# Performance work log

Hardware: AMD Instinct MI355X
Metric: run time of the kernel (lower is better)

Reference implementation:

```python
import jax, jax.numpy as jnp
import numpy as np

K_NEIGHBORS = 8  # hard-coded k in extract_edge_features
NUM_HEADS = 12


def _sqdist(a, b):
    # a [B,M,3], b [B,N,3] -> squared euclidean distances [B,M,N]
    # (monotone in cdist, so argmax/top-k indices are identical to torch.cdist)
    return jnp.sum((a[:, :, None, :] - b[:, None, :, :]) ** 2, axis=-1)


def _fps(points, num_samples):
    # Farthest point sampling (intended semantics of farthest_point_sampling):
    # iteratively pick the point maximizing the min distance to the selected set.
    B, N, _ = points.shape
    bidx = jnp.arange(B)

    def d_to(idx):  # idx [B] -> squared dist from points[b, idx[b]] to all points [B,N]
        p = points[bidx, idx]  # [B,3]
        return jnp.sum((points - p[:, None, :]) ** 2, axis=-1)

    idx0 = jnp.zeros((B,), jnp.int32)  # deterministic start point

    def step(min_d, _):
        nxt = jnp.argmax(min_d, axis=-1).astype(jnp.int32)  # [B]
        min_d = jnp.minimum(min_d, d_to(nxt))
        return min_d, nxt

    _, rest = jax.lax.scan(step, d_to(idx0), None, length=num_samples - 1)  # rest [M-1,B]
    idxs = jnp.concatenate([idx0[None, :], rest], axis=0).T  # [B,M]
    return jnp.take_along_axis(points, idxs[:, :, None], axis=1)  # [B,M,3]


def _edge_features(points, features, k=K_NEIGHBORS):
    # EdgeAligner.extract_edge_features: kNN by cdist+topk(smallest), then
    # edge = feature - mean(neighbor features)
    d2 = _sqdist(points, points)  # [B,M,M]
    _, nn_idx = jax.lax.top_k(-d2, k)  # [B,M,k] indices of k nearest (incl. self)
    nbr = jax.vmap(lambda f, idx: f[idx])(features, nn_idx)  # [B,M,k,D]
    return features - jnp.mean(nbr, axis=2)


def _mha(x, Wq, bq, Wk, bk, Wv, bv, Wo, bo, num_heads=NUM_HEADS):
    # standard torch nn.MultiheadAttention (self-attention, batch_first)
    B, S, D = x.shape
    dh = D // num_heads
    split = lambda t: t.reshape(B, S, num_heads, dh).transpose(0, 2, 1, 3)
    q = split(x @ Wq + bq)
    k = split(x @ Wk + bk)
    v = split(x @ Wv + bv)
    scale = jnp.asarray(1.0 / np.sqrt(dh), x.dtype)
    att = jax.nn.softmax(jnp.einsum('bhqd,bhkd->bhqk', q, k) * scale, axis=-1)
    o = jnp.einsum('bhqk,bhkd->bhqd', att, v)  # [B,H,S,dh]
    o = o.transpose(0, 2, 1, 3).reshape(B, S, D)
    return o @ Wo + bo


def setup_inputs() -> dict:
    key = jax.random.key(0)
    ks = jax.random.split(key, 8)
    B, N, D = 4, 8192, 768
    s = 0.02
    return {
        'points': jax.random.normal(ks[0], (B, N, 3), jnp.float32),
        'W_embed': jax.random.normal(ks[1], (3, D), jnp.float32) * s,
        'b_embed': jnp.zeros((D,), jnp.float32),
        'Wq': jax.random.normal(ks[2], (D, D), jnp.float32) * s,
        'bq': jnp.zeros((D,), jnp.float32),
        'Wk': jax.random.normal(ks[3], (D, D), jnp.float32) * s,
        'bk': jnp.zeros((D,), jnp.float32),
        'Wv': jax.random.normal(ks[4], (D, D), jnp.float32) * s,
        'bv': jnp.zeros((D,), jnp.float32),
        'Wo': jax.random.normal(ks[5], (D, D), jnp.float32) * s,
        'bo': jnp.zeros((D,), jnp.float32),
        'Ws': jax.random.normal(ks[6], (3, D), jnp.float32) * s,
        'bs': jnp.zeros((D,), jnp.float32),
        'num_samples': 1024,
    }


def reference(points, W_embed, b_embed, Wq, bq, Wk, bk, Wv, bv, Wo, bo, Ws, bs, num_samples):
    # 1) farthest point sampling N -> M
    sampled = _fps(points, num_samples)  # [B,M,3]
    # 2) point embedding (point_embed: Linear(3, 768))
    feats = sampled @ W_embed + b_embed  # [B,M,768]
    # 3) EdgeAligner forward with no external neighbor subsets:
    #    edge features -> self bi-attention -> + spatial embedding
    edge = _edge_features(sampled, feats)  # [B,M,768]
    aligned = _mha(edge, Wq, bq, Wk, bk, Wv, bv, Wo, bo)  # [B,M,768]
    spatial = sampled @ Ws + bs  # spatial_embed: Linear(3, 768)
    return aligned + spatial
```

## Files before the change

kernel.cpp:

```cpp
#include <hip/hip_runtime.h>
#include <float.h>
#include <math.h>

#define BB   4
#define NPTS 8192
#define MS   1024
#define DIM  768
#define NH   12
#define DHD  64
#define KNN  8
#define BMD  (BB*MS*DIM)

static __device__ __forceinline__ float sqdist3(float ax, float ay, float az,
                                                float bx, float by, float bz) {
  float dx = __fsub_rn(ax, bx);
  float dy = __fsub_rn(ay, by);
  float dz = __fsub_rn(az, bz);
  return __fadd_rn(__fadd_rn(__fmul_rn(dx, dx), __fmul_rn(dy, dy)), __fmul_rn(dz, dz));
}

__global__ __launch_bounds__(1024) void fps_kernel(const float* __restrict__ points,
                                                   float* __restrict__ sampled) {
  const int b = blockIdx.x;
  const float* pts = points + (size_t)b * NPTS * 3;
  float* smp = sampled + (size_t)b * MS * 3;
  const int tid = threadIdx.x;
  const int lane = tid & 63, wid = tid >> 6;

  __shared__ float cxs[NPTS], cys[NPTS], czs[NPTS];
  __shared__ unsigned long long red[2][16];

  float px[8], py[8], pz[8], md[8];
  const float qx0 = pts[0], qy0 = pts[1], qz0 = pts[2];
#pragma unroll
  for (int j = 0; j < 8; ++j) {
    int i = tid + j * 1024;
    float x = pts[i * 3 + 0], y = pts[i * 3 + 1], z = pts[i * 3 + 2];
    px[j] = x; py[j] = y; pz[j] = z;
    cxs[i] = x; cys[i] = y; czs[i] = z;
    md[j] = sqdist3(x, y, z, qx0, qy0, qz0);
  }
  if (tid == 0) { smp[0] = qx0; smp[1] = qy0; smp[2] = qz0; }
  __syncthreads();

  for (int s = 1; s < MS; ++s) {
    float bv = md[0]; int bj = 0;
#pragma unroll
    for (int j = 1; j < 8; ++j)
      if (md[j] > bv) { bv = md[j]; bj = j; }
    unsigned long long key =
        ((unsigned long long)__float_as_uint(bv) << 32) |
        (unsigned)(~(unsigned)(tid + bj * 1024));

#pragma unroll
    for (int off = 1; off < 64; off <<= 1) {
      unsigned long long ok = __shfl_xor(key, off);
      if (ok > key) key = ok;
    }
    const int buf = s & 1;
    if (lane == 0) red[buf][wid] = key;
    __syncthreads();

    unsigned long long kk[16];
#pragma unroll
    for (int i = 0; i < 16; ++i) kk[i] = red[buf][i];
#pragma unroll
    for (int st = 8; st >= 1; st >>= 1)
#pragma unroll
      for (int i = 0; i < 8; ++i)
        if (i < st && kk[i + st] > kk[i]) kk[i] = kk[i + st];

    const unsigned widx = ~(unsigned)(kk[0] & 0xffffffffull);
    const float wx = cxs[widx], wy = cys[widx], wz = czs[widx];
    if (tid == 0) {
      smp[s * 3 + 0] = wx; smp[s * 3 + 1] = wy; smp[s * 3 + 2] = wz;
    }
#pragma unroll
    for (int j = 0; j < 8; ++j) {
      float d = sqdist3(px[j], py[j], pz[j], wx, wy, wz);
      md[j] = fminf(md[j], d);
    }
  }
}

__global__ void embed_kernel(const float* __restrict__ sampled,
                             const float* __restrict__ W,
                             const float* __restrict__ bias,
                             float* __restrict__ out) {
  int idx = blockIdx.x * blockDim.x + threadIdx.x;
  if (idx >= BMD) return;
  int d = idx % DIM;
  int bm = idx / DIM;
  float x = sampled[bm * 3 + 0], y = sampled[bm * 3 + 1], z = sampled[bm * 3 + 2];
  out[idx] = fmaf(z, W[2 * DIM + d], fmaf(y, W[DIM + d], fmaf(x, W[d], bias[d])));
}

__global__ __launch_bounds__(256) void knn_edge_kernel(const float* __restrict__ sampled,
                                                       const float* __restrict__ feats,
                                                       float* __restrict__ edge) {
  const int bm = blockIdx.x;
  const int b = bm >> 10, m = bm & 1023;
  const float* sp = sampled + (size_t)b * MS * 3;
  const int t = threadIdx.x, lane = t & 63, wid = t >> 6;

  __shared__ float dist[MS];
  __shared__ float redv[4];
  __shared__ int   redi[4];
  __shared__ int   win[KNN];

  const float qx = sp[m * 3 + 0], qy = sp[m * 3 + 1], qz = sp[m * 3 + 2];
#pragma unroll
  for (int j = 0; j < 4; ++j) {
    int i = t + j * 256;
    dist[i] = sqdist3(sp[i * 3 + 0], sp[i * 3 + 1], sp[i * 3 + 2], qx, qy, qz);
  }
  __syncthreads();

  for (int it = 0; it < KNN; ++it) {
    float bv = dist[t]; int bi = t;
#pragma unroll
    for (int j = 1; j < 4; ++j) {
      int i = t + j * 256;
      float v = dist[i];
      if (v < bv || (v == bv && i < bi)) { bv = v; bi = i; }
    }
#pragma unroll
    for (int off = 32; off >= 1; off >>= 1) {
      float ov = __shfl_xor(bv, off);
      int   oi = __shfl_xor(bi, off);
      if (ov < bv || (ov == bv && oi < bi)) { bv = ov; bi = oi; }
    }
    if (lane == 0) { redv[wid] = bv; redi[wid] = bi; }
    __syncthreads();
    if (t == 0) {
      float wv = redv[0]; int wi = redi[0];
#pragma unroll
      for (int w = 1; w < 4; ++w) {
        float ov = redv[w]; int oi = redi[w];
        if (ov < wv || (ov == wv && oi < wi)) { wv = ov; wi = oi; }
      }
      win[it] = wi;
      dist[wi] = FLT_MAX;
    }
    __syncthreads();
  }

  const float* fb = feats + (size_t)b * MS * DIM;
  float* eb = edge + (size_t)b * MS * DIM;
  for (int d = t; d < DIM; d += 256) {
    float acc = 0.f;
#pragma unroll
    for (int i = 0; i < KNN; ++i) acc += fb[(size_t)win[i] * DIM + d];
    eb[(size_t)m * DIM + d] = fb[(size_t)m * DIM + d] - acc * 0.125f;
  }
}

template <int MODE>
__global__ __launch_bounds__(256) void gemm_kernel(const float* __restrict__ A,
                                                   const float* __restrict__ W,
                                                   const float* __restrict__ bias,
                                                   float* __restrict__ C,
                                                   const float* __restrict__ sampled,
                                                   const float* __restrict__ Ws,
                                                   const float* __restrict__ bs) {
  __shared__ float As[16][68];
  __shared__ float Bs[16][68];

  const int t = threadIdx.x;
  const int tx = t & 15, ty = t >> 4;
  const int rowBase = blockIdx.x * 64;
  const int nBase = blockIdx.y * 64;

  float c[4][4] = {};

  const int ar = t >> 2, ac4 = (t & 3) * 4;
  const int br = t >> 4, bc4 = (t & 15) * 4;

  for (int k0 = 0; k0 < DIM; k0 += 16) {
    float4 a = *(const float4*)&A[(size_t)(rowBase + ar) * DIM + k0 + ac4];
    As[ac4 + 0][ar] = a.x; As[ac4 + 1][ar] = a.y;
    As[ac4 + 2][ar] = a.z; As[ac4 + 3][ar] = a.w;
    float4 w = *(const float4*)&W[(size_t)(k0 + br) * DIM + nBase + bc4];
    *(float4*)&Bs[br][bc4] = w;
    __syncthreads();
#pragma unroll
    for (int k = 0; k < 16; ++k) {
      float av[4], bv[4];
      *(float4*)av = *(const float4*)&As[k][ty * 4];
      *(float4*)bv = *(const float4*)&Bs[k][tx * 4];
#pragma unroll
      for (int i = 0; i < 4; ++i)
#pragma unroll
        for (int j = 0; j < 4; ++j)
          c[i][j] = fmaf(av[i], bv[j], c[i][j]);
    }
    __syncthreads();
  }

#pragma unroll
  for (int i = 0; i < 4; ++i) {
    int row = rowBase + ty * 4 + i;
#pragma unroll
    for (int j = 0; j < 4; ++j) {
      int n = nBase + tx * 4 + j;
      float v = c[i][j] + bias[n];
      if (MODE == 1) {
        const float* sp = sampled + (size_t)row * 3;
        float spt = fmaf(sp[2], Ws[2 * DIM + n], fmaf(sp[1], Ws[DIM + n], fmaf(sp[0], Ws[n], bs[n])));
        v += spt;
      }
      C[(size_t)row * DIM + n] = v;
    }
  }
}

static __device__ __forceinline__ int lidx(int r, int c) {
  return r * 64 + (c ^ ((r & 7) << 2));
}

__global__ __launch_bounds__(256) void attn_kernel(const float* __restrict__ Q,
                                                   const float* __restrict__ K,
                                                   const float* __restrict__ V,
                                                   float* __restrict__ O) {
  const int nrt = MS / 64;
  const int blk = blockIdx.x;
  const int bh = blk / nrt, rt = blk % nrt;
  const int b = bh / NH, h = bh % NH;
  const int t = threadIdx.x, lane = t & 63, w = t >> 6;
  const int rg = lane >> 4, kg = lane & 15;

  __shared__ float Qs[64 * 64];
  __shared__ float Ks[64 * 64];
  __shared__ float Vs[64 * 64];
  __shared__ float Ps[4 * 16 * 64];

  const size_t base = (size_t)(b * MS) * DIM + (size_t)h * DHD;

#pragma unroll
  for (int i = 0; i < 4; ++i) {
    int f = t + i * 256;
    int r = f >> 4, c4 = (f & 15) * 4;
    *(float4*)&Qs[lidx(r, c4)] = *(const float4*)&Q[base + (size_t)(rt * 64 + r) * DIM + c4];
  }

  float m[4], l[4], o[4][4];
#pragma unroll
  for (int i = 0; i < 4; ++i) {
    m[i] = -INFINITY; l[i] = 0.f;
#pragma unroll
    for (int j = 0; j < 4; ++j) o[i][j] = 0.f;
  }

  const int lrow = w * 16 + rg * 4;
  float* Pw = &Ps[w * 16 * 64];

  for (int kt = 0; kt < nrt; ++kt) {
#pragma unroll
    for (int i = 0; i < 4; ++i) {
      int f = t + i * 256;
      int r = f >> 4, c4 = (f & 15) * 4;
      size_t g = base + (size_t)(kt * 64 + r) * DIM + c4;
      *(float4*)&Ks[lidx(r, c4)] = *(const float4*)&K[g];
      *(float4*)&Vs[lidx(r, c4)] = *(const float4*)&V[g];
    }
    __syncthreads();

    float s[4][4] = {};
#pragma unroll 8
    for (int d = 0; d < 64; ++d) {
      float a[4], bb[4];
#pragma unroll
      for (int i = 0; i < 4; ++i) a[i] = Qs[lidx(lrow + i, d)];
#pragma unroll
      for (int j = 0; j < 4; ++j) bb[j] = Ks[lidx(kg + 16 * j, d)];
#pragma unroll
      for (int i = 0; i < 4; ++i)
#pragma unroll
        for (int j = 0; j < 4; ++j) s[i][j] = fmaf(a[i], bb[j], s[i][j]);
    }

#pragma unroll
    for (int i = 0; i < 4; ++i) {
#pragma unroll
      for (int j = 0; j < 4; ++j) s[i][j] *= 0.125f;
      float mt = fmaxf(fmaxf(s[i][0], s[i][1]), fmaxf(s[i][2], s[i][3]));
#pragma unroll
      for (int off = 1; off < 16; off <<= 1) mt = fmaxf(mt, __shfl_xor(mt, off));
      float mn = fmaxf(m[i], mt);
      float corr = expf(m[i] - mn);
      float ps = 0.f;
#pragma unroll
      for (int j = 0; j < 4; ++j) { s[i][j] = expf(s[i][j] - mn); ps += s[i][j]; }
#pragma unroll
      for (int off = 1; off < 16; off <<= 1) ps += __shfl_xor(ps, off);
      l[i] = l[i] * corr + ps;
      m[i] = mn;
#pragma unroll
      for (int j = 0; j < 4; ++j) o[i][j] *= corr;
#pragma unroll
      for (int j = 0; j < 4; ++j) Pw[lidx(rg * 4 + i, kg + 16 * j)] = s[i][j];
    }

#pragma unroll 8
    for (int k = 0; k < 64; ++k) {
      float a[4], bb[4];
#pragma unroll
      for (int i = 0; i < 4; ++i) a[i] = Pw[lidx(rg * 4 + i, k)];
#pragma unroll
      for (int j = 0; j < 4; ++j) bb[j] = Vs[lidx(k, kg + 16 * j)];
#pragma unroll
      for (int i = 0; i < 4; ++i)
#pragma unroll
        for (int j = 0; j < 4; ++j) o[i][j] = fmaf(a[i], bb[j], o[i][j]);
    }
    __syncthreads();
  }

#pragma unroll
  for (int i = 0; i < 4; ++i) {
    int row = rt * 64 + lrow + i;
#pragma unroll
    for (int j = 0; j < 4; ++j)
      O[base + (size_t)row * DIM + kg + 16 * j] = o[i][j] / l[i];
  }
}

extern "C" void kernel_launch(void* const* d_in, const int* in_sizes, int n_in,
                              void* d_out, int out_size, void* d_ws, size_t ws_size,
                              hipStream_t stream) {
  const float* points  = (const float*)d_in[0];
  const float* W_embed = (const float*)d_in[1];
  const float* b_embed = (const float*)d_in[2];
  const float* Wq = (const float*)d_in[3];
  const float* bq = (const float*)d_in[4];
  const float* Wk = (const float*)d_in[5];
  const float* bk = (const float*)d_in[6];
  const float* Wv = (const float*)d_in[7];
  const float* bv = (const float*)d_in[8];
  const float* Wo = (const float*)d_in[9];
  const float* bo = (const float*)d_in[10];
  const float* Ws = (const float*)d_in[11];
  const float* bs = (const float*)d_in[12];

  float* ws = (float*)d_ws;
  float* sampled = ws;
  float* feats   = ws + 16384;
  float* edge    = feats + BMD;
  float* qb      = edge + BMD;
  float* kb      = qb + BMD;
  float* vb      = kb + BMD;
  float* ao      = vb + BMD;

  fps_kernel<<<BB, 1024, 0, stream>>>(points, sampled);
  embed_kernel<<<(BMD + 255) / 256, 256, 0, stream>>>(sampled, W_embed, b_embed, feats);
  knn_edge_kernel<<<BB * MS, 256, 0, stream>>>(sampled, feats, edge);

  dim3 ggrid(4096 / 64, DIM / 64);
  gemm_kernel<0><<<ggrid, 256, 0, stream>>>(edge, Wq, bq, qb, nullptr, nullptr, nullptr);
  gemm_kernel<0><<<ggrid, 256, 0, stream>>>(edge, Wk, bk, kb, nullptr, nullptr, nullptr);
  gemm_kernel<0><<<ggrid, 256, 0, stream>>>(edge, Wv, bv, vb, nullptr, nullptr, nullptr);

  attn_kernel<<<BB * NH * (MS / 64), 256, 0, stream>>>(qb, kb, vb, ao);

  gemm_kernel<1><<<ggrid, 256, 0, stream>>>(ao, Wo, bo, (float*)d_out, sampled, Ws, bs);
}
```

Before: 2.091 ms.

## Shrink FPS block to 4 waves with DPP reductions, enlarge GEMM row tile

The farthest-point-sampling kernel now runs 256 threads per batch, each holding 32 points. The argmax is fused into the distance-update loop, and the wave reduction uses DPP row/broadcast ops instead of shuffles. Coordinates are packed as float4 in shared memory, and the cross-wave reduction shrinks from 16 entries to 4, which cuts per-iteration barrier and reduction latency on the serial 1023-step loop. Separately, the generic GEMM tile grows from 64x64 to 128x64 with an 8x4 per-thread micro-tile. This halves the grid and raises register use for more reuse per load.

Result: faster. 1.833 ms (-12.4%).

```diff
diff --git a/kernel.cpp b/kernel.cpp
--- a/kernel.cpp
+++ b/kernel.cpp
@@ -19,66 +19,82 @@
   return __fadd_rn(__fadd_rn(__fmul_rn(dx, dx), __fmul_rn(dy, dy)), __fmul_rn(dz, dz));
 }
 
-__global__ __launch_bounds__(1024) void fps_kernel(const float* __restrict__ points,
-                                                   float* __restrict__ sampled) {
+#define DPP_STAGE(key, ctrl)                                                   \
+  {                                                                            \
+    unsigned hi_ = (unsigned)((key) >> 32), lo_ = (unsigned)(key);             \
+    unsigned nhi_ = (unsigned)__builtin_amdgcn_update_dpp(                     \
+        (int)hi_, (int)hi_, (ctrl), 0xf, 0xf, false);                          \
+    unsigned nlo_ = (unsigned)__builtin_amdgcn_update_dpp(                     \
+        (int)lo_, (int)lo_, (ctrl), 0xf, 0xf, false);                          \
+    unsigned long long nk_ = ((unsigned long long)nhi_ << 32) | nlo_;          \
+    if (nk_ > (key)) (key) = nk_;                                              \
+  }
+
+__global__ __launch_bounds__(256, 1) void fps_kernel(const float* __restrict__ points,
+                                                     float* __restrict__ sampled) {
   const int b = blockIdx.x;
   const float* pts = points + (size_t)b * NPTS * 3;
   float* smp = sampled + (size_t)b * MS * 3;
   const int tid = threadIdx.x;
-  const int lane = tid & 63, wid = tid >> 6;
-
-  __shared__ float cxs[NPTS], cys[NPTS], czs[NPTS];
-  __shared__ unsigned long long red[2][16];
-
-  float px[8], py[8], pz[8], md[8];
+  const int lane = tid & 63, w = tid >> 6;
+
+  __shared__ float4 cxyz[NPTS];
+  __shared__ unsigned long long red[2][4];
+
+  float px[32], py[32], pz[32], md[32];
   const float qx0 = pts[0], qy0 = pts[1], qz0 = pts[2];
-#pragma unroll
-  for (int j = 0; j < 8; ++j) {
-    int i = tid + j * 1024;
+
+  float bv = -INFINITY;
+  int bidx = 0;
+#pragma unroll
+  for (int j = 0; j < 32; ++j) {
+    int i = tid + j * 256;
     float x = pts[i * 3 + 0], y = pts[i * 3 + 1], z = pts[i * 3 + 2];
     px[j] = x; py[j] = y; pz[j] = z;
-    cxs[i] = x; cys[i] = y; czs[i] = z;
-    md[j] = sqdist3(x, y, z, qx0, qy0, qz0);
+    cxyz[i] = make_float4(x, y, z, 0.f);
+    float d = sqdist3(x, y, z, qx0, qy0, qz0);
+    md[j] = d;
+    if (d > bv) { bv = d; bidx = i; }
   }
   if (tid == 0) { smp[0] = qx0; smp[1] = qy0; smp[2] = qz0; }
   __syncthreads();
 
   for (int s = 1; s < MS; ++s) {
-    float bv = md[0]; int bj = 0;
-#pragma unroll
-    for (int j = 1; j < 8; ++j)
-      if (md[j] > bv) { bv = md[j]; bj = j; }
     unsigned long long key =
         ((unsigned long long)__float_as_uint(bv) << 32) |
-        (unsigned)(~(unsigned)(tid + bj * 1024));
-
-#pragma unroll
-    for (int off = 1; off < 64; off <<= 1) {
-      unsigned long long ok = __shfl_xor(key, off);
-      if (ok > key) key = ok;
-    }
+        (unsigned)(~(unsigned)bidx);
+
+    DPP_STAGE(key, 0xB1);
+    DPP_STAGE(key, 0x4E);
+    DPP_STAGE(key, 0x141);
+    DPP_STAGE(key, 0x140);
+    DPP_STAGE(key, 0x142);
+    DPP_STAGE(key, 0x143);
+
     const int buf = s & 1;
-    if (lane == 0) red[buf][wid] = key;
-    __syncthreads();
-
-    unsigned long long kk[16];
-#pragma unroll
-    for (int i = 0; i < 16; ++i) kk[i] = red[buf][i];
-#pragma unroll
-    for (int st = 8; st >= 1; st >>= 1)
-#pragma unroll
-      for (int i = 0; i < 8; ++i)
-        if (i < st && kk[i + st] > kk[i]) kk[i] = kk[i + st];
-
-    const unsigned widx = ~(unsigned)(kk[0] & 0xffffffffull);
-    const float wx = cxs[widx], wy = cys[widx], wz = czs[widx];
+    if (lane == 63) red[buf][w] = key;
+    __syncthreads();
+
+    unsigned long long k0 = red[buf][0], k1 = red[buf][1];
+    unsigned long long k2 = red[buf][2], k3 = red[buf][3];
+    unsigned long long a = (k0 > k1) ? k0 : k1;
+    unsigned long long c = (k2 > k3) ? k2 : k3;
+    unsigned long long fk = (a > c) ? a : c;
+    const unsigned widx = ~(unsigned)(fk & 0xffffffffull);
+
+    const float4 wc = cxyz[widx];
     if (tid == 0) {
-      smp[s * 3 + 0] = wx; smp[s * 3 + 1] = wy; smp[s * 3 + 2] = wz;
-    }
-#pragma unroll
-    for (int j = 0; j < 8; ++j) {
-      float d = sqdist3(px[j], py[j], pz[j], wx, wy, wz);
-      md[j] = fminf(md[j], d);
+      smp[s * 3 + 0] = wc.x; smp[s * 3 + 1] = wc.y; smp[s * 3 + 2] = wc.z;
+    }
+
+    bv = -INFINITY; bidx = 0;
+#pragma unroll
+    for (int j = 0; j < 32; ++j) {
+      int i = tid + j * 256;
+      float d = sqdist3(px[j], py[j], pz[j], wc.x, wc.y, wc.z);
+      float nm = fminf(md[j], d);
+      md[j] = nm;
+      if (nm > bv) { bv = nm; bidx = i; }
     }
   }
 }
@@ -163,33 +179,37 @@
                                                    const float* __restrict__ sampled,
                                                    const float* __restrict__ Ws,
                                                    const float* __restrict__ bs) {
-  __shared__ float As[16][68];
+  __shared__ float As[16][132];
   __shared__ float Bs[16][68];
 
   const int t = threadIdx.x;
   const int tx = t & 15, ty = t >> 4;
-  const int rowBase = blockIdx.x * 64;
+  const int rowBase = blockIdx.x * 128;
   const int nBase = blockIdx.y * 64;
 
-  float c[4][4] = {};
-
-  const int ar = t >> 2, ac4 = (t & 3) * 4;
+  float c[8][4] = {};
+
+  const int ar = t >> 1, ac8 = (t & 1) * 8;
   const int br = t >> 4, bc4 = (t & 15) * 4;
 
   for (int k0 = 0; k0 < DIM; k0 += 16) {
-    float4 a = *(const float4*)&A[(size_t)(rowBase + ar) * DIM + k0 + ac4];
-    As[ac4 + 0][ar] = a.x; As[ac4 + 1][ar] = a.y;
-    As[ac4 + 2][ar] = a.z; As[ac4 + 3][ar] = a.w;
-    float4 w = *(const float4*)&W[(size_t)(k0 + br) * DIM + nBase + bc4];
-    *(float4*)&Bs[br][bc4] = w;
+    float4 a0 = *(const float4*)&A[(size_t)(rowBase + ar) * DIM + k0 + ac8];
+    float4 a1 = *(const float4*)&A[(size_t)(rowBase + ar) * DIM + k0 + ac8 + 4];
+    As[ac8 + 0][ar] = a0.x; As[ac8 + 1][ar] = a0.y;
+    As[ac8 + 2][ar] = a0.z; As[ac8 + 3][ar] = a0.w;
+    As[ac8 + 4][ar] = a1.x; As[ac8 + 5][ar] = a1.y;
+    As[ac8 + 6][ar] = a1.z; As[ac8 + 7][ar] = a1.w;
+    float4 wv = *(const float4*)&W[(size_t)(k0 + br) * DIM + nBase + bc4];
+    *(float4*)&Bs[br][bc4] = wv;
     __syncthreads();
 #pragma unroll
     for (int k = 0; k < 16; ++k) {
-      float av[4], bv[4];
-      *(float4*)av = *(const float4*)&As[k][ty * 4];
+      float av[8], bv[4];
+      *(float4*)&av[0] = *(const float4*)&As[k][ty * 8];
+      *(float4*)&av[4] = *(const float4*)&As[k][ty * 8 + 4];
       *(float4*)bv = *(const float4*)&Bs[k][tx * 4];
 #pragma unroll
-      for (int i = 0; i < 4; ++i)
+      for (int i = 0; i < 8; ++i)
 #pragma unroll
         for (int j = 0; j < 4; ++j)
           c[i][j] = fmaf(av[i], bv[j], c[i][j]);
@@ -198,8 +218,8 @@
   }
 
 #pragma unroll
-  for (int i = 0; i < 4; ++i) {
-    int row = rowBase + ty * 4 + i;
+  for (int i = 0; i < 8; ++i) {
+    int row = rowBase + ty * 8 + i;
 #pragma unroll
     for (int j = 0; j < 4; ++j) {
       int n = nBase + tx * 4 + j;
@@ -351,11 +371,11 @@
   float* vb      = kb + BMD;
   float* ao      = vb + BMD;
 
-  fps_kernel<<<BB, 1024, 0, stream>>>(points, sampled);
+  fps_kernel<<<BB, 256, 0, stream>>>(points, sampled);
   embed_kernel<<<(BMD + 255) / 256, 256, 0, stream>>>(sampled, W_embed, b_embed, feats);
   knn_edge_kernel<<<BB * MS, 256, 0, stream>>>(sampled, feats, edge);
 
-  dim3 ggrid(4096 / 64, DIM / 64);
+  dim3 ggrid(4096 / 128, DIM / 64);
   gemm_kernel<0><<<ggrid, 256, 0, stream>>>(edge, Wq, bq, qb, nullptr, nullptr, nullptr);
   gemm_kernel<0><<<ggrid, 256, 0, stream>>>(edge, Wk, bk, kb, nullptr, nullptr, nullptr);
   gemm_kernel<0><<<ggrid, 256, 0, stream>>>(edge, Wv, bv, vb, nullptr, nullptr, nullptr);
```
